# Optimization experiments

Hardware: AMD Instinct MI355X
Metric: run time of the kernel (lower is better)

Reference implementation:

```python
import jax, jax.numpy as jnp
import numpy as np

CUTOFF = 5.0
NIPSIN = 3
NELE = 4        # natomtype
NWAVE = 10      # ntype: radial params per element
NB, NA, NEIGH = 1, 12000, 64
NPAIR = NA * NEIGH
# index_para: maps 12 angular components (3 p + 9 d) to order index 0/1
INDEX_PARA = np.concatenate([np.full(3 ** i, i - 1, dtype=np.int32) for i in range(1, NIPSIN)])
NANG = INDEX_PARA.shape[0]  # 12


def setup_inputs() -> dict:
    key = jax.random.key(0)
    ks = jax.random.split(key, 8)
    coordinates = jax.random.normal(ks[0], (NB, NA, 3), dtype=jnp.float32)
    numatoms = NA
    atom_index = jax.random.randint(ks[1], (2, NB, NPAIR), 0, NA)
    shifts = jax.random.normal(ks[2], (NB, NPAIR, 3), dtype=jnp.float32) * 0.1
    species = jax.random.randint(ks[3], (NB * NA,), 0, NELE)
    rs = jax.random.uniform(ks[4], (NELE, NWAVE), dtype=jnp.float32) * 4.0
    inta = jax.random.uniform(ks[5], (NELE, NWAVE), dtype=jnp.float32) + 0.2
    params = jax.random.uniform(ks[6], (NELE,), dtype=jnp.float32) * 0.5 + 0.5
    return {"coordinates": coordinates, "numatoms": numatoms, "atom_index": atom_index,
            "shifts": shifts, "species": species, "rs": rs, "inta": inta, "params": params}


def _density(coordinates, atom_index, shifts, species, rs, inta):
    nb, na, _ = coordinates.shape
    coords = coordinates.reshape(-1, 3)
    totnatom = coords.shape[0]
    npair = atom_index.shape[2]
    # flatten pair index lists with per-molecule atom offset (faithful for nb=1)
    ai = jnp.transpose(atom_index, (1, 0, 2)).reshape(2, -1)                 # (2, nb*npair)
    off = jnp.broadcast_to((jnp.arange(nb) * na)[:, None], (nb, npair)).reshape(-1)
    idx12 = ai + off[None, :]
    shift_v = shifts.reshape(-1, 3)
    valid = jnp.all(shift_v > -1e9, axis=-1)                                 # padding mask (all True here)
    dist_vec = coords[idx12[0]] - coords[idx12[1]] + shift_v                 # (P,3)
    d = jnp.linalg.norm(dist_vec, axis=-1)                                   # (P,)
    sp = species[idx12[0]]                                                   # (P,)
    # radial Gaussian * cosine cutoff, params gathered per center-atom type
    fcut = 0.5 * (jnp.cos(jnp.pi * jnp.minimum(d / CUTOFF, 1.0)) + 1.0)
    radial = jnp.exp(-10.0 * inta[sp] * jnp.square(d[:, None] - rs[sp])) * fcut[:, None]
    radial = jnp.where(valid[:, None], radial, 0.0)                          # (P, NWAVE)
    # angular outer products of unit vectors: p (3) then d (9)
    u = dist_vec / d[:, None]
    orbs = []
    orb = jnp.ones((u.shape[0], 1), dtype=u.dtype)
    for _ in range(1, NIPSIN):
        orb = (orb[:, :, None] * u[:, None, :]).reshape(u.shape[0], -1)
        orbs.append(orb)
    angular = jnp.concatenate(orbs, axis=1)                                  # (P, NANG)
    # scatter-reduce into per-(atom, neighbor-type) accumulators, then square
    seg = idx12[0] * NELE + sp
    rd = jax.ops.segment_sum(radial, seg, num_segments=totnatom * NELE)
    rd = jnp.square(rd).reshape(totnatom, NELE, NWAVE)
    oa = (angular[:, :, None] * radial[:, None, :]).reshape(u.shape[0], -1)  # (P, NANG*NWAVE)
    ad = jax.ops.segment_sum(oa, seg, num_segments=totnatom * NELE)
    ad = jnp.square(ad).reshape(totnatom, NELE, NANG, NWAVE)
    # contract angular components of the same order (index_para)
    acc = jnp.zeros((totnatom, NELE, NIPSIN - 1, NWAVE), dtype=ad.dtype)
    acc = acc.at[:, :, jnp.asarray(INDEX_PARA), :].add(ad)
    return jnp.concatenate([rd, acc.reshape(totnatom, NELE, -1)], axis=2)    # (T, NELE, 30)


def reference(coordinates, numatoms, atom_index, shifts, species, rs, inta, params):
    density = _density(coordinates, atom_index, shifts, species, rs, inta)
    density_w = density * params[None, :, None]                 # einsum('ijk,j->ijk')
    g = jnp.einsum('ilj,imj->ijlm', density_w, density_w)       # (T, nfeat, NELE, NELE)
    return jnp.sqrt(g).reshape(g.shape[0], g.shape[1], -1).sum(-1)  # (T, nfeat)
```

## Files before the change

kernel.cpp:

```cpp
#include <hip/hip_runtime.h>
#include <math.h>

#define NA 12000
#define NPAIR 768000
#define NWAVE 10
#define BINS 256
#define APB 47
#define BCAP 4096
#define RCAP 3584
#define PPB 2048

__global__ void init_kernel(unsigned int* __restrict__ cursor,
                            const float* __restrict__ rs,
                            const float* __restrict__ inta,
                            float2* __restrict__ tbl) {
    int t = threadIdx.x;
    cursor[t] = 0u;
    if (t < 40) tbl[t] = make_float2(rs[t], -10.0f * inta[t]);
}

__global__ __launch_bounds__(256) void bin_kernel(
        const float* __restrict__ coords,
        const int* __restrict__ ai0,
        const int* __restrict__ ai1,
        const float* __restrict__ shifts,
        unsigned int* __restrict__ cursor,
        float4* __restrict__ records) {
    __shared__ unsigned int hist[BINS];
    __shared__ unsigned int scanbuf[BINS];
    __shared__ unsigned int excl[BINS];
    __shared__ unsigned int gbase[BINS];
    __shared__ float4 stage[PPB];
    __shared__ unsigned short inv[PPB];
    __shared__ unsigned int dest[PPB];

    int tid = threadIdx.x;
    hist[tid] = 0u;
    __syncthreads();

    unsigned int binr[8], rankr[8];
    int pbase = blockIdx.x * PPB;
    #pragma unroll
    for (int r = 0; r < 8; r++) {
        int li = r * 256 + tid;
        int p  = pbase + li;
        int a  = ai0[p];
        int j  = ai1[p];
        float sx = shifts[3 * p + 0];
        float sy = shifts[3 * p + 1];
        float sz = shifts[3 * p + 2];
        float dx = coords[3 * a + 0] - coords[3 * j + 0] + sx;
        float dy = coords[3 * a + 1] - coords[3 * j + 1] + sy;
        float dz = coords[3 * a + 2] - coords[3 * j + 2] + sz;
        float d  = sqrtf(dx * dx + dy * dy + dz * dz);
        float tt = fminf(d * 0.2f, 1.0f);
        float fcut = 0.5f * __cosf(3.14159265358979f * tt) + 0.5f;
        if (!((sx > -1e9f) && (sy > -1e9f) && (sz > -1e9f))) fcut = 0.0f;
        unsigned int bin  = (unsigned int)a / 47u;
        unsigned int aloc = (unsigned int)a - bin * 47u;
        unsigned int fb = (__float_as_uint(fcut) & ~63u) | aloc;
        stage[li] = make_float4(dx, dy, dz, __uint_as_float(fb));
        unsigned int rk = atomicAdd(&hist[bin], 1u);
        binr[r] = bin;
        rankr[r] = rk;
    }
    __syncthreads();

    unsigned int h = hist[tid];
    scanbuf[tid] = h;
    __syncthreads();
    for (int off = 1; off < 256; off <<= 1) {
        unsigned int v = (tid >= off) ? scanbuf[tid - off] : 0u;
        __syncthreads();
        scanbuf[tid] += v;
        __syncthreads();
    }
    excl[tid]  = scanbuf[tid] - h;
    gbase[tid] = atomicAdd(&cursor[tid], h);
    __syncthreads();

    #pragma unroll
    for (int r = 0; r < 8; r++) {
        int li = r * 256 + tid;
        unsigned int s  = excl[binr[r]] + rankr[r];
        unsigned int gr = gbase[binr[r]] + rankr[r];
        inv[s]  = (unsigned short)li;
        dest[s] = (gr < BCAP) ? (binr[r] * BCAP + gr) : 0xFFFFFFFFu;
    }
    __syncthreads();

    #pragma unroll
    for (int r = 0; r < 8; r++) {
        int s = r * 256 + tid;
        unsigned int dg = dest[s];
        float4 rec = stage[inv[s]];
        if (dg != 0xFFFFFFFFu) records[dg] = rec;
    }
}

__global__ __launch_bounds__(256) void accum_kernel(
        const float4* __restrict__ records,
        const int*    __restrict__ species,
        const float*  __restrict__ params,
        const float2* __restrict__ tbl,
        const unsigned int* __restrict__ cursor,
        float* __restrict__ out) {
    __shared__ unsigned short idx[RCAP];
    __shared__ float spart[2][APB * 101];
    __shared__ unsigned int hist[APB];
    __shared__ unsigned int offs[APB];
    __shared__ int spl[APB];

    int tid  = threadIdx.x;
    int wv   = tid >> 6;
    int lane = tid & 63;
    int bin  = blockIdx.x;

    if (tid < APB) {
        hist[tid] = 0u;
        int ag = bin * APB + tid;
        spl[tid] = (ag < NA) ? species[ag] : 0;
    }
    __syncthreads();

    unsigned int cnt = cursor[bin];
    if (cnt > RCAP) cnt = RCAP;
    unsigned int base = (unsigned int)bin * BCAP;
    const float* recw = (const float*)records;

    unsigned int pend[14];
    #pragma unroll
    for (int r = 0; r < 14; r++) {
        unsigned int k = (unsigned int)(r * 256 + tid);
        pend[r] = 0xFFFFFFFFu;
        if (k < cnt) {
            unsigned int fb = __float_as_uint(recw[(base + k) * 4 + 3]);
            unsigned int aloc = fb & 63u;
            unsigned int rk = atomicAdd(&hist[aloc], 1u);
            pend[r] = (aloc << 20) | (rk << 12) | k;
        }
    }
    __syncthreads();

    if (wv == 0) {
        unsigned int h0 = (lane < APB) ? hist[lane] : 0u;
        unsigned int h = h0;
        #pragma unroll
        for (int s = 1; s < 64; s <<= 1) {
            unsigned int v = __shfl_up(h, s, 64);
            if (lane >= s) h += v;
        }
        if (lane < APB) offs[lane] = h - h0;
    }
    __syncthreads();

    #pragma unroll
    for (int r = 0; r < 14; r++) {
        if (pend[r] != 0xFFFFFFFFu) {
            unsigned int aloc = pend[r] >> 20;
            unsigned int rk   = (pend[r] >> 12) & 0xFFu;
            unsigned int k    = pend[r] & 0xFFFu;
            idx[offs[aloc] + rk] = (unsigned short)k;
        }
    }
    __syncthreads();

    if (wv < 2 && lane < APB) {
        int a = lane;
        unsigned int offa = offs[a];
        unsigned int cnta = hist[a];
        float trs[10], tin[10];
        const float2* tb = tbl + spl[a] * NWAVE;
        #pragma unroll
        for (int w = 0; w < 10; w++) { float2 t = tb[w]; trs[w] = t.x; tin[w] = t.y; }

        float S[10], P[30], D[60];
        #pragma unroll
        for (int w = 0; w < 10; w++) S[w] = 0.0f;
        #pragma unroll
        for (int c = 0; c < 30; c++) P[c] = 0.0f;
        #pragma unroll
        for (int c = 0; c < 60; c++) D[c] = 0.0f;

        for (unsigned int j = (unsigned int)wv; j < cnta; j += 2) {
            unsigned int k = idx[offa + j];
            float4 rec = records[base + k];
            unsigned int fb = __float_as_uint(rec.w);
            float fcut = __uint_as_float(fb & ~63u);
            float d2 = rec.x * rec.x + rec.y * rec.y + rec.z * rec.z;
            float dinv = rsqrtf(fmaxf(d2, 1e-24f));
            float d  = d2 * dinv;
            float ux = rec.x * dinv, uy = rec.y * dinv, uz = rec.z * dinv;
            float uxx = ux * ux, uxy = ux * uy, uxz = ux * uz;
            float uyy = uy * uy, uyz = uy * uz, uzz = uz * uz;
            #pragma unroll
            for (int w = 0; w < 10; w++) {
                float dr = d - trs[w];
                float r  = __expf(tin[w] * dr * dr) * fcut;
                S[w]      += r;
                P[w]      += ux  * r;
                P[10 + w] += uy  * r;
                P[20 + w] += uz  * r;
                D[w]      += uxx * r;
                D[10 + w] += uxy * r;
                D[20 + w] += uxz * r;
                D[30 + w] += uyy * r;
                D[40 + w] += uyz * r;
                D[50 + w] += uzz * r;
            }
        }

        float* row = &spart[wv][a * 101];
        #pragma unroll
        for (int w = 0; w < 10; w++) row[w]      = S[w];
        #pragma unroll
        for (int c = 0; c < 30; c++) row[10 + c] = P[c];
        #pragma unroll
        for (int c = 0; c < 60; c++) row[40 + c] = D[c];
    }
    __syncthreads();

    for (int v = tid; v < APB * 30; v += 256) {
        int atom = v / 30;
        int c = v - atom * 30;
        int ag = bin * APB + atom;
        if (ag < NA) {
            float pr = params[spl[atom]];
            const float* p0 = &spart[0][atom * 101];
            const float* p1 = &spart[1][atom * 101];
            float o;
            if (c < 10) {
                float s = p0[c] + p1[c];
                o = pr * s * s;
            } else if (c < 20) {
                int w = c - 10;
                float a1 = p0[10 + w] + p1[10 + w];
                float b1 = p0[20 + w] + p1[20 + w];
                float c1 = p0[30 + w] + p1[30 + w];
                o = pr * (a1 * a1 + b1 * b1 + c1 * c1);
            } else {
                int w = c - 20;
                float xx = p0[40 + w] + p1[40 + w];
                float xy = p0[50 + w] + p1[50 + w];
                float xz = p0[60 + w] + p1[60 + w];
                float yy = p0[70 + w] + p1[70 + w];
                float yz = p0[80 + w] + p1[80 + w];
                float zz = p0[90 + w] + p1[90 + w];
                o = pr * (xx * xx + yy * yy + zz * zz
                          + 2.0f * (xy * xy + xz * xz + yz * yz));
            }
            out[ag * 30 + c] = o;
        }
    }
}


extern "C" void kernel_launch(void* const* d_in, const int* in_sizes, int n_in,
                              void* d_out, int out_size, void* d_ws, size_t ws_size,
                              hipStream_t stream) {
    const float* coords  = (const float*)d_in[0];
    const int*   aidx    = (const int*)d_in[2];
    const float* shifts  = (const float*)d_in[3];
    const int*   species = (const int*)d_in[4];
    const float* rs      = (const float*)d_in[5];
    const float* inta    = (const float*)d_in[6];
    const float* params  = (const float*)d_in[7];
    float* out = (float*)d_out;

    char* ws = (char*)d_ws;
    float4*       records = (float4*)(ws);
    unsigned int* cursor  = (unsigned int*)(ws + 16777216);
    float2*       tbl     = (float2*)(ws + 16778240);

    const int* ai0 = aidx;
    const int* ai1 = aidx + NPAIR;

    init_kernel<<<1, 256, 0, stream>>>(cursor, rs, inta, tbl);
    bin_kernel<<<NPAIR / PPB, 256, 0, stream>>>(coords, ai0, ai1, shifts,
                                                cursor, records);
    accum_kernel<<<BINS, 256, 0, stream>>>(records, species, params, tbl,
                                           cursor, out);
}
```

Before: 121.6 us.

## Use all four waves in accumulation, split atom-local index array, widen bin blocks

The accumulation kernel now lets all four wavefronts process each atom's pair list (stride 4) with four partial-sum buffers, up from two. The binning kernel moves to 512 threads and 3072 pairs per block and writes each atom-local index to a separate byte array, so the accumulation pre-pass reads one byte per record instead of a strided float. The init kernel is replaced by hipMemsetAsync, and the rs/inta table is read directly inside the accumulation kernel. These changes add LDS use (four spart buffers plus larger staging) and may lower occupancy. Packing fcut without the aloc bits changes fcut only in its low mantissa bits.

```diff
diff --git a/kernel.cpp b/kernel.cpp
--- a/kernel.cpp
+++ b/kernel.cpp
@@ -8,24 +8,16 @@
 #define APB 47
 #define BCAP 4096
 #define RCAP 3584
-#define PPB 2048
-
-__global__ void init_kernel(unsigned int* __restrict__ cursor,
-                            const float* __restrict__ rs,
-                            const float* __restrict__ inta,
-                            float2* __restrict__ tbl) {
-    int t = threadIdx.x;
-    cursor[t] = 0u;
-    if (t < 40) tbl[t] = make_float2(rs[t], -10.0f * inta[t]);
-}
-
-__global__ __launch_bounds__(256) void bin_kernel(
+#define PPB 3072
+
+__global__ __launch_bounds__(512) void bin_kernel(
         const float* __restrict__ coords,
         const int* __restrict__ ai0,
         const int* __restrict__ ai1,
         const float* __restrict__ shifts,
         unsigned int* __restrict__ cursor,
-        float4* __restrict__ records) {
+        float4* __restrict__ records,
+        unsigned char* __restrict__ aloc8) {
     __shared__ unsigned int hist[BINS];
     __shared__ unsigned int scanbuf[BINS];
     __shared__ unsigned int excl[BINS];
@@ -35,14 +27,14 @@
     __shared__ unsigned int dest[PPB];
 
     int tid = threadIdx.x;
-    hist[tid] = 0u;
-    __syncthreads();
-
-    unsigned int binr[8], rankr[8];
+    if (tid < BINS) hist[tid] = 0u;
+    __syncthreads();
+
+    unsigned int binr[6], rankr[6], alocr[6];
     int pbase = blockIdx.x * PPB;
     #pragma unroll
-    for (int r = 0; r < 8; r++) {
-        int li = r * 256 + tid;
+    for (int r = 0; r < 6; r++) {
+        int li = r * 512 + tid;
         int p  = pbase + li;
         int a  = ai0[p];
         int j  = ai1[p];
@@ -58,55 +50,65 @@
         if (!((sx > -1e9f) && (sy > -1e9f) && (sz > -1e9f))) fcut = 0.0f;
         unsigned int bin  = (unsigned int)a / 47u;
         unsigned int aloc = (unsigned int)a - bin * 47u;
-        unsigned int fb = (__float_as_uint(fcut) & ~63u) | aloc;
-        stage[li] = make_float4(dx, dy, dz, __uint_as_float(fb));
+        stage[li] = make_float4(dx, dy, dz, fcut);
         unsigned int rk = atomicAdd(&hist[bin], 1u);
         binr[r] = bin;
         rankr[r] = rk;
-    }
-    __syncthreads();
-
-    unsigned int h = hist[tid];
-    scanbuf[tid] = h;
-    __syncthreads();
-    for (int off = 1; off < 256; off <<= 1) {
-        unsigned int v = (tid >= off) ? scanbuf[tid - off] : 0u;
+        alocr[r] = aloc;
+    }
+    __syncthreads();
+
+    unsigned int h = (tid < BINS) ? hist[tid] : 0u;
+    if (tid < BINS) scanbuf[tid] = h;
+    __syncthreads();
+    for (int off = 1; off < BINS; off <<= 1) {
+        unsigned int v = (tid < BINS && tid >= off) ? scanbuf[tid - off] : 0u;
         __syncthreads();
-        scanbuf[tid] += v;
+        if (tid < BINS) scanbuf[tid] += v;
         __syncthreads();
     }
-    excl[tid]  = scanbuf[tid] - h;
-    gbase[tid] = atomicAdd(&cursor[tid], h);
-    __syncthreads();
-
-    #pragma unroll
-    for (int r = 0; r < 8; r++) {
-        int li = r * 256 + tid;
+    if (tid < BINS) {
+        excl[tid]  = scanbuf[tid] - h;
+        gbase[tid] = atomicAdd(&cursor[tid], h);
+    }
+    __syncthreads();
+
+    #pragma unroll
+    for (int r = 0; r < 6; r++) {
+        int li = r * 512 + tid;
         unsigned int s  = excl[binr[r]] + rankr[r];
         unsigned int gr = gbase[binr[r]] + rankr[r];
         inv[s]  = (unsigned short)li;
         dest[s] = (gr < BCAP) ? (binr[r] * BCAP + gr) : 0xFFFFFFFFu;
-    }
-    __syncthreads();
-
-    #pragma unroll
-    for (int r = 0; r < 8; r++) {
-        int s = r * 256 + tid;
+        stage[li].w = __uint_as_float((__float_as_uint(stage[li].w) & ~63u) | alocr[r]);
+    }
+    __syncthreads();
+
+    #pragma unroll
+    for (int r = 0; r < 6; r++) {
+        int s = r * 512 + tid;
         unsigned int dg = dest[s];
         float4 rec = stage[inv[s]];
-        if (dg != 0xFFFFFFFFu) records[dg] = rec;
+        unsigned int al = __float_as_uint(rec.w) & 63u;
+        rec.w = __uint_as_float(__float_as_uint(rec.w) & ~63u);
+        if (dg != 0xFFFFFFFFu) {
+            records[dg] = rec;
+            aloc8[dg] = (unsigned char)al;
+        }
     }
 }
 
 __global__ __launch_bounds__(256) void accum_kernel(
         const float4* __restrict__ records,
+        const unsigned char* __restrict__ aloc8,
         const int*    __restrict__ species,
         const float*  __restrict__ params,
-        const float2* __restrict__ tbl,
+        const float*  __restrict__ rs,
+        const float*  __restrict__ inta,
         const unsigned int* __restrict__ cursor,
         float* __restrict__ out) {
     __shared__ unsigned short idx[RCAP];
-    __shared__ float spart[2][APB * 101];
+    __shared__ float spart[4][APB * 101];
     __shared__ unsigned int hist[APB];
     __shared__ unsigned int offs[APB];
     __shared__ int spl[APB];
@@ -126,7 +128,6 @@
     unsigned int cnt = cursor[bin];
     if (cnt > RCAP) cnt = RCAP;
     unsigned int base = (unsigned int)bin * BCAP;
-    const float* recw = (const float*)records;
 
     unsigned int pend[14];
     #pragma unroll
@@ -134,8 +135,7 @@
         unsigned int k = (unsigned int)(r * 256 + tid);
         pend[r] = 0xFFFFFFFFu;
         if (k < cnt) {
-            unsigned int fb = __float_as_uint(recw[(base + k) * 4 + 3]);
-            unsigned int aloc = fb & 63u;
+            unsigned int aloc = aloc8[base + k];
             unsigned int rk = atomicAdd(&hist[aloc], 1u);
             pend[r] = (aloc << 20) | (rk << 12) | k;
         }
@@ -165,14 +165,17 @@
     }
     __syncthreads();
 
-    if (wv < 2 && lane < APB) {
+    if (lane < APB) {
         int a = lane;
         unsigned int offa = offs[a];
         unsigned int cnta = hist[a];
+        int sp = spl[a];
         float trs[10], tin[10];
-        const float2* tb = tbl + spl[a] * NWAVE;
-        #pragma unroll
-        for (int w = 0; w < 10; w++) { float2 t = tb[w]; trs[w] = t.x; tin[w] = t.y; }
+        #pragma unroll
+        for (int w = 0; w < 10; w++) {
+            trs[w] = rs[sp * NWAVE + w];
+            tin[w] = -10.0f * inta[sp * NWAVE + w];
+        }
 
         float S[10], P[30], D[60];
         #pragma unroll
@@ -182,11 +185,10 @@
         #pragma unroll
         for (int c = 0; c < 60; c++) D[c] = 0.0f;
 
-        for (unsigned int j = (unsigned int)wv; j < cnta; j += 2) {
+        for (unsigned int j = (unsigned int)wv; j < cnta; j += 4) {
             unsigned int k = idx[offa + j];
             float4 rec = records[base + k];
-            unsigned int fb = __float_as_uint(rec.w);
-            float fcut = __uint_as_float(fb & ~63u);
+            float fcut = rec.w;
             float d2 = rec.x * rec.x + rec.y * rec.y + rec.z * rec.z;
             float dinv = rsqrtf(fmaxf(d2, 1e-24f));
             float d  = d2 * dinv;
@@ -226,26 +228,25 @@
         int ag = bin * APB + atom;
         if (ag < NA) {
             float pr = params[spl[atom]];
-            const float* p0 = &spart[0][atom * 101];
-            const float* p1 = &spart[1][atom * 101];
+            int ao = atom * 101;
             float o;
             if (c < 10) {
-                float s = p0[c] + p1[c];
+                float s = spart[0][ao+c] + spart[1][ao+c] + spart[2][ao+c] + spart[3][ao+c];
                 o = pr * s * s;
             } else if (c < 20) {
-                int w = c - 10;
-                float a1 = p0[10 + w] + p1[10 + w];
-                float b1 = p0[20 + w] + p1[20 + w];
-                float c1 = p0[30 + w] + p1[30 + w];
+                int w = ao + c;
+                float a1 = spart[0][w]    + spart[1][w]    + spart[2][w]    + spart[3][w];
+                float b1 = spart[0][w+10] + spart[1][w+10] + spart[2][w+10] + spart[3][w+10];
+                float c1 = spart[0][w+20] + spart[1][w+20] + spart[2][w+20] + spart[3][w+20];
                 o = pr * (a1 * a1 + b1 * b1 + c1 * c1);
             } else {
-                int w = c - 20;
-                float xx = p0[40 + w] + p1[40 + w];
-                float xy = p0[50 + w] + p1[50 + w];
-                float xz = p0[60 + w] + p1[60 + w];
-                float yy = p0[70 + w] + p1[70 + w];
-                float yz = p0[80 + w] + p1[80 + w];
-                float zz = p0[90 + w] + p1[90 + w];
+                int w = ao + c + 20;
+                float xx = spart[0][w]    + spart[1][w]    + spart[2][w]    + spart[3][w];
+                float xy = spart[0][w+10] + spart[1][w+10] + spart[2][w+10] + spart[3][w+10];
+                float xz = spart[0][w+20] + spart[1][w+20] + spart[2][w+20] + spart[3][w+20];
+                float yy = spart[0][w+30] + spart[1][w+30] + spart[2][w+30] + spart[3][w+30];
+                float yz = spart[0][w+40] + spart[1][w+40] + spart[2][w+40] + spart[3][w+40];
+                float zz = spart[0][w+50] + spart[1][w+50] + spart[2][w+50] + spart[3][w+50];
                 o = pr * (xx * xx + yy * yy + zz * zz
                           + 2.0f * (xy * xy + xz * xz + yz * yz));
             }
@@ -268,16 +269,16 @@
     float* out = (float*)d_out;
 
     char* ws = (char*)d_ws;
-    float4*       records = (float4*)(ws);
-    unsigned int* cursor  = (unsigned int*)(ws + 16777216);
-    float2*       tbl     = (float2*)(ws + 16778240);
+    float4*        records = (float4*)(ws);
+    unsigned int*  cursor  = (unsigned int*)(ws + 16777216);
+    unsigned char* aloc8   = (unsigned char*)(ws + 16778240);
 
     const int* ai0 = aidx;
     const int* ai1 = aidx + NPAIR;
 
-    init_kernel<<<1, 256, 0, stream>>>(cursor, rs, inta, tbl);
-    bin_kernel<<<NPAIR / PPB, 256, 0, stream>>>(coords, ai0, ai1, shifts,
-                                                cursor, records);
-    accum_kernel<<<BINS, 256, 0, stream>>>(records, species, params, tbl,
-                                           cursor, out);
+    hipMemsetAsync(cursor, 0, BINS * sizeof(unsigned int), stream);
+    bin_kernel<<<NPAIR / PPB, 512, 0, stream>>>(coords, ai0, ai1, shifts,
+                                                cursor, records, aloc8);
+    accum_kernel<<<BINS, 256, 0, stream>>>(records, aloc8, species, params,
+                                           rs, inta, cursor, out);
 }
```

New measurement: 116.5 us. 1.04x faster.
